# Kernel optimization log

Hardware: AMD Instinct MI355X
Metric: run time of the kernel (lower is better)

The kernel has to match this reference:

```python
import jax, jax.numpy as jnp
import numpy as np

N_DRUG, N_TARGET, N_EDGES, H = 50000, 20000, 500000, 256


def setup_inputs() -> dict:
    key = jax.random.key(0)
    ks = jax.random.split(key, 6)
    s = 1.0 / np.sqrt(2 * H)
    return {
        "z_drug": jax.random.normal(ks[0], (N_DRUG, H), dtype=jnp.float32),
        "z_target": jax.random.normal(ks[1], (N_TARGET, H), dtype=jnp.float32),
        "row": jax.random.randint(ks[2], (N_EDGES,), 0, N_DRUG, dtype=jnp.int64),
        "col": jax.random.randint(ks[3], (N_EDGES,), 0, N_TARGET, dtype=jnp.int64),
        "W1": jax.random.normal(ks[4], (2 * H, H), dtype=jnp.float32) * s,
        "b1": jnp.zeros((H,), dtype=jnp.float32),
        "W2": jax.random.normal(ks[5], (H, 1), dtype=jnp.float32) * (1.0 / np.sqrt(H)),
        "b2": jnp.zeros((1,), dtype=jnp.float32),
    }


def reference(z_drug, z_target, row, col, W1, b1, W2, b2):
    # gather endpoint embeddings by edge index, concat -> [E, 2H]
    zc = jnp.concatenate([z_drug[row], z_target[col]], axis=-1)
    h = jax.nn.relu(zc @ W1 + b1)          # [E, H]
    return h @ W2 + b2                     # [E, 1]
```

## Files before the change

### kernel.cpp

```cpp
#include <hip/hip_runtime.h>
#include <hip/hip_bf16.h>
#include <stdint.h>


typedef unsigned short u16;
typedef __attribute__((ext_vector_type(8))) short short8;
typedef __attribute__((ext_vector_type(4))) float f32x4;

#define HDIM 256
#define KDIM 512
#define BM 128
#define BK 64

__device__ __forceinline__ u16 f2bf(float f) {
  union { float f; uint32_t u; } v; v.f = f;
  uint32_t u = v.u;
  return (u16)((u + 0x7fffu + ((u >> 16) & 1u)) >> 16);
}

__device__ __forceinline__ void gl2lds16(const void* g, void* l) {
  __builtin_amdgcn_global_load_lds(
      (const __attribute__((address_space(1))) unsigned int*)g,
      (__attribute__((address_space(3))) unsigned int*)l,
      16, 0, 0);
}

#define CVT_BLOCKS 4096
__global__ void prep_kernel(const float* __restrict__ zd_f,
                            const float* __restrict__ zt_f,
                            const float* __restrict__ w1,
                            u16* __restrict__ zdb, u16* __restrict__ ztb,
                            u16* __restrict__ w1t, int n4d, int n4t) {
  const int b = blockIdx.x;
  if (b < 32) {
    __shared__ float tile[64][65];
    const int k0 = (b >> 2) * 64, n0 = (b & 3) * 64;
    const int tx = threadIdx.x & 63, ty = threadIdx.x >> 6;
#pragma unroll
    for (int i = ty; i < 64; i += 4)
      tile[i][tx] = w1[(size_t)(k0 + i) * HDIM + n0 + tx];
    __syncthreads();
#pragma unroll
    for (int i = ty; i < 64; i += 4)
      w1t[(size_t)(n0 + i) * KDIM + k0 + tx] = f2bf(tile[tx][i]);
  } else {
    const int idx = (b - 32) * 256 + threadIdx.x;
    const int stride = CVT_BLOCKS * 256;
    for (int i = idx; i < n4d; i += stride) {
      float4 v = ((const float4*)zd_f)[i];
      ushort4 o; o.x = f2bf(v.x); o.y = f2bf(v.y); o.z = f2bf(v.z); o.w = f2bf(v.w);
      ((ushort4*)zdb)[i] = o;
    }
    for (int i = idx; i < n4t; i += stride) {
      float4 v = ((const float4*)zt_f)[i];
      ushort4 o; o.x = f2bf(v.x); o.y = f2bf(v.y); o.z = f2bf(v.z); o.w = f2bf(v.w);
      ((ushort4*)ztb)[i] = o;
    }
  }
}

__global__ __launch_bounds__(256, 2) void edge_mlp_kernel(
    const u16* __restrict__ zd, const u16* __restrict__ zt,
    const int* __restrict__ row, const int* __restrict__ col,
    const u16* __restrict__ w1t, const float* __restrict__ b1,
    const float* __restrict__ w2, const float* __restrict__ b2,
    float* __restrict__ out, int E) {
  __shared__ u16 lB[2][HDIM * BK];

  const int tid   = threadIdx.x;
  const int wid   = tid >> 6;
  const int lane  = tid & 63;
  const int e0    = blockIdx.x * BM;
  const int r8    = lane >> 3;
  const int slog  = ((lane & 7) ^ (r8 & 7)) * 8;
  const int colid = lane & 15;
  const int quad  = lane >> 4;
  const int csw   = colid & 7;

  const u16* pB = w1t + (uint32_t)(wid * 64 + r8) * KDIM + slog;

  uint32_t offD2[2], offT2[2];
#pragma unroll
  for (int rt = 0; rt < 2; ++rt) {
    int ge = min(e0 + wid * 32 + rt * 16 + colid, E - 1);
    offD2[rt] = (uint32_t)row[ge] * HDIM;
    offT2[rt] = (uint32_t)col[ge] * HDIM;
  }

  f32x4 acc[2][16];
#pragma unroll
  for (int i = 0; i < 2; ++i)
#pragma unroll
    for (int j = 0; j < 16; ++j) acc[i][j] = f32x4{0.f, 0.f, 0.f, 0.f};

  short8 aR[2][2][2];

#pragma unroll
  for (int j = 0; j < 8; ++j)
    gl2lds16(pB + (size_t)j * 8 * KDIM, &lB[0][(wid * 64 + j * 8) * BK]);
#pragma unroll
  for (int rt = 0; rt < 2; ++rt)
#pragma unroll
    for (int s = 0; s < 2; ++s)
      aR[0][rt][s] = *(const short8*)(zd + offD2[rt] + s * 32 + quad * 8);
  asm volatile("s_waitcnt vmcnt(0)" ::: "memory");
  __builtin_amdgcn_s_barrier();

#pragma unroll
  for (int kc = 0; kc < 8; ++kc) {
    const int cur = kc & 1, nxt = cur ^ 1;
    if (kc < 7) {
      const int kn = kc + 1;
      const u16* zb = (kn < 4) ? zd : zt;
      const uint32_t* offs = (kn < 4) ? offD2 : offT2;
      const int koffn = (kn & 3) * BK;
#pragma unroll
      for (int j = 0; j < 8; ++j)
        gl2lds16(pB + (size_t)j * 8 * KDIM + kn * BK,
                 &lB[nxt][(wid * 64 + j * 8) * BK]);
#pragma unroll
      for (int rt = 0; rt < 2; ++rt)
#pragma unroll
        for (int s = 0; s < 2; ++s)
          aR[nxt][rt][s] =
              *(const short8*)(zb + offs[rt] + koffn + s * 32 + quad * 8);
    }
#pragma unroll
    for (int s = 0; s < 2; ++s) {
      const int sl = s * 4 + quad;
      __builtin_amdgcn_s_setprio(1);
#pragma unroll
      for (int ct = 0; ct < 16; ++ct) {
        short8 bF = *(const short8*)
            &lB[cur][(ct * 16 + colid) * BK + ((sl ^ csw) * 8)];
        acc[0][ct] = __builtin_amdgcn_mfma_f32_16x16x32_bf16(
            aR[cur][0][s], bF, acc[0][ct], 0, 0, 0);
        acc[1][ct] = __builtin_amdgcn_mfma_f32_16x16x32_bf16(
            aR[cur][1][s], bF, acc[1][ct], 0, 0, 0);
      }
      __builtin_amdgcn_s_setprio(0);
    }
    if (kc < 7) {
      asm volatile("s_waitcnt vmcnt(0)" ::: "memory");
      __builtin_amdgcn_s_barrier();
    }
  }

  float b1v[16], w2v[16];
#pragma unroll
  for (int ct = 0; ct < 16; ++ct) {
    b1v[ct] = b1[ct * 16 + colid];
    w2v[ct] = w2[ct * 16 + colid];
  }
  const float b2v = b2[0];
#pragma unroll
  for (int rt = 0; rt < 2; ++rt)
#pragma unroll
    for (int j = 0; j < 4; ++j) {
      float s = 0.f;
#pragma unroll
      for (int ct = 0; ct < 16; ++ct)
        s += fmaxf(acc[rt][ct][j] + b1v[ct], 0.f) * w2v[ct];
#pragma unroll
      for (int off = 8; off >= 1; off >>= 1)
        s += __shfl_xor(s, off, 16);
      if (colid == 0) {
        int ge = e0 + wid * 32 + rt * 16 + quad * 4 + j;
        if (ge < E) out[ge] = s + b2v;
      }
    }
}

__global__ void fallback_kernel(
    const float* __restrict__ zd, const float* __restrict__ zt,
    const int* __restrict__ row, const int* __restrict__ col,
    const float* __restrict__ W1, const float* __restrict__ b1,
    const float* __restrict__ W2, const float* __restrict__ b2,
    float* __restrict__ out, int E) {
  __shared__ float zc[16][512];
  __shared__ float red[4][16];
  const int e0 = blockIdx.x * 16;
  const int tid = threadIdx.x;
  for (int i = tid; i < 16 * 512; i += 256) {
    int e = i >> 9, k = i & 511;
    int ge = min(e0 + e, E - 1);
    zc[e][k] = (k < HDIM) ? zd[(size_t)row[ge] * HDIM + k]
                          : zt[(size_t)col[ge] * HDIM + (k - HDIM)];
  }
  __syncthreads();
  float acc[16];
#pragma unroll
  for (int e = 0; e < 16; ++e) acc[e] = 0.f;
  for (int k = 0; k < KDIM; ++k) {
    float w = W1[k * HDIM + tid];
#pragma unroll
    for (int e = 0; e < 16; ++e) acc[e] += zc[e][k] * w;
  }
  float wv = W2[tid], bv = b1[tid];
  const int lane = tid & 63, wid = tid >> 6;
#pragma unroll
  for (int e = 0; e < 16; ++e) {
    float pv = fmaxf(acc[e] + bv, 0.f) * wv;
#pragma unroll
    for (int off = 32; off >= 1; off >>= 1) pv += __shfl_down(pv, off, 64);
    if (lane == 0) red[wid][e] = pv;
  }
  __syncthreads();
  if (tid < 16) {
    int ge = e0 + tid;
    if (ge < E)
      out[ge] = red[0][tid] + red[1][tid] + red[2][tid] + red[3][tid] + b2[0];
  }
}

extern "C" void kernel_launch(void* const* d_in, const int* in_sizes, int n_in,
                              void* d_out, int out_size, void* d_ws, size_t ws_size,
                              hipStream_t stream) {
  const float* zd_f = (const float*)d_in[0];
  const float* zt_f = (const float*)d_in[1];
  const int*   row  = (const int*)d_in[2];
  const int*   col  = (const int*)d_in[3];
  const float* W1   = (const float*)d_in[4];
  const float* b1   = (const float*)d_in[5];
  const float* W2   = (const float*)d_in[6];
  const float* b2   = (const float*)d_in[7];
  float* out = (float*)d_out;

  const int E  = in_sizes[2];
  const int ND = in_sizes[0] / HDIM;
  const int NT = in_sizes[1] / HDIM;

  size_t off_w1t = 0;
  size_t off_zd  = (size_t)KDIM * HDIM * sizeof(u16);
  size_t off_zt  = off_zd + (size_t)ND * HDIM * sizeof(u16);
  size_t need    = off_zt + (size_t)NT * HDIM * sizeof(u16);

  if (ws_size >= need) {
    u16* w1t = (u16*)((char*)d_ws + off_w1t);
    u16* zdb = (u16*)((char*)d_ws + off_zd);
    u16* ztb = (u16*)((char*)d_ws + off_zt);
    int n4d = ND * HDIM / 4, n4t = NT * HDIM / 4;
    prep_kernel<<<32 + CVT_BLOCKS, 256, 0, stream>>>(zd_f, zt_f, W1,
                                                     zdb, ztb, w1t, n4d, n4t);
    edge_mlp_kernel<<<(E + BM - 1) / BM, 256, 0, stream>>>(
        zdb, ztb, row, col, w1t, b1, W2, b2, out, E);
  } else {
    fallback_kernel<<<(E + 15) / 16, 256, 0, stream>>>(
        zd_f, zt_f, row, col, W1, b1, W2, b2, out, E);
  }
}
```

Measured before the change: 265.9 us.

## Fuse fp32-to-bf16 embedding conversion into edge MLP gather

Removes the separate pass that converted both embedding tables to bf16 in workspace; the edge kernel now gathers fp32 rows directly and converts to bf16 in registers after the load wait. This eliminates a full read/write sweep of the tables. In exchange, the per-edge gather traffic doubles and more registers are used to hold the fp32 staging values.

```diff
diff --git a/kernel.cpp b/kernel.cpp
--- a/kernel.cpp
+++ b/kernel.cpp
@@ -25,42 +25,23 @@
       16, 0, 0);
 }
 
-#define CVT_BLOCKS 4096
-__global__ void prep_kernel(const float* __restrict__ zd_f,
-                            const float* __restrict__ zt_f,
-                            const float* __restrict__ w1,
-                            u16* __restrict__ zdb, u16* __restrict__ ztb,
-                            u16* __restrict__ w1t, int n4d, int n4t) {
+__global__ void prep_kernel(const float* __restrict__ w1,
+                            u16* __restrict__ w1t) {
   const int b = blockIdx.x;
-  if (b < 32) {
-    __shared__ float tile[64][65];
-    const int k0 = (b >> 2) * 64, n0 = (b & 3) * 64;
-    const int tx = threadIdx.x & 63, ty = threadIdx.x >> 6;
-#pragma unroll
-    for (int i = ty; i < 64; i += 4)
-      tile[i][tx] = w1[(size_t)(k0 + i) * HDIM + n0 + tx];
-    __syncthreads();
-#pragma unroll
-    for (int i = ty; i < 64; i += 4)
-      w1t[(size_t)(n0 + i) * KDIM + k0 + tx] = f2bf(tile[tx][i]);
-  } else {
-    const int idx = (b - 32) * 256 + threadIdx.x;
-    const int stride = CVT_BLOCKS * 256;
-    for (int i = idx; i < n4d; i += stride) {
-      float4 v = ((const float4*)zd_f)[i];
-      ushort4 o; o.x = f2bf(v.x); o.y = f2bf(v.y); o.z = f2bf(v.z); o.w = f2bf(v.w);
-      ((ushort4*)zdb)[i] = o;
-    }
-    for (int i = idx; i < n4t; i += stride) {
-      float4 v = ((const float4*)zt_f)[i];
-      ushort4 o; o.x = f2bf(v.x); o.y = f2bf(v.y); o.z = f2bf(v.z); o.w = f2bf(v.w);
-      ((ushort4*)ztb)[i] = o;
-    }
-  }
+  __shared__ float tile[64][65];
+  const int k0 = (b >> 2) * 64, n0 = (b & 3) * 64;
+  const int tx = threadIdx.x & 63, ty = threadIdx.x >> 6;
+#pragma unroll
+  for (int i = ty; i < 64; i += 4)
+    tile[i][tx] = w1[(size_t)(k0 + i) * HDIM + n0 + tx];
+  __syncthreads();
+#pragma unroll
+  for (int i = ty; i < 64; i += 4)
+    w1t[(size_t)(n0 + i) * KDIM + k0 + tx] = f2bf(tile[tx][i]);
 }
 
 __global__ __launch_bounds__(256, 2) void edge_mlp_kernel(
-    const u16* __restrict__ zd, const u16* __restrict__ zt,
+    const float* __restrict__ zdf, const float* __restrict__ ztf,
     const int* __restrict__ row, const int* __restrict__ col,
     const u16* __restrict__ w1t, const float* __restrict__ b1,
     const float* __restrict__ w2, const float* __restrict__ b2,
@@ -93,17 +74,43 @@
 #pragma unroll
     for (int j = 0; j < 16; ++j) acc[i][j] = f32x4{0.f, 0.f, 0.f, 0.f};
 
-  short8 aR[2][2][2];
+  float4 a32[2][2][2];
+  short8 aB[2][2];
+
+  auto loadA = [&](int kn) {
+    const float* zb = (kn < 4) ? zdf : ztf;
+    const uint32_t* offs = (kn < 4) ? offD2 : offT2;
+    const int koffn = (kn & 3) * BK;
+#pragma unroll
+    for (int rt = 0; rt < 2; ++rt)
+#pragma unroll
+      for (int s = 0; s < 2; ++s) {
+        const float* p = zb + offs[rt] + koffn + s * 32 + quad * 8;
+        a32[rt][s][0] = ((const float4*)p)[0];
+        a32[rt][s][1] = ((const float4*)p)[1];
+      }
+  };
+  auto cvtA = [&]() {
+#pragma unroll
+    for (int rt = 0; rt < 2; ++rt)
+#pragma unroll
+      for (int s = 0; s < 2; ++s) {
+        float4 lo = a32[rt][s][0], hi = a32[rt][s][1];
+        short8 r;
+        r[0] = (short)f2bf(lo.x); r[1] = (short)f2bf(lo.y);
+        r[2] = (short)f2bf(lo.z); r[3] = (short)f2bf(lo.w);
+        r[4] = (short)f2bf(hi.x); r[5] = (short)f2bf(hi.y);
+        r[6] = (short)f2bf(hi.z); r[7] = (short)f2bf(hi.w);
+        aB[rt][s] = r;
+      }
+  };
 
 #pragma unroll
   for (int j = 0; j < 8; ++j)
     gl2lds16(pB + (size_t)j * 8 * KDIM, &lB[0][(wid * 64 + j * 8) * BK]);
-#pragma unroll
-  for (int rt = 0; rt < 2; ++rt)
-#pragma unroll
-    for (int s = 0; s < 2; ++s)
-      aR[0][rt][s] = *(const short8*)(zd + offD2[rt] + s * 32 + quad * 8);
+  loadA(0);
   asm volatile("s_waitcnt vmcnt(0)" ::: "memory");
+  cvtA();
   __builtin_amdgcn_s_barrier();
 
 #pragma unroll
@@ -111,19 +118,11 @@
     const int cur = kc & 1, nxt = cur ^ 1;
     if (kc < 7) {
       const int kn = kc + 1;
-      const u16* zb = (kn < 4) ? zd : zt;
-      const uint32_t* offs = (kn < 4) ? offD2 : offT2;
-      const int koffn = (kn & 3) * BK;
 #pragma unroll
       for (int j = 0; j < 8; ++j)
         gl2lds16(pB + (size_t)j * 8 * KDIM + kn * BK,
                  &lB[nxt][(wid * 64 + j * 8) * BK]);
-#pragma unroll
-      for (int rt = 0; rt < 2; ++rt)
-#pragma unroll
-        for (int s = 0; s < 2; ++s)
-          aR[nxt][rt][s] =
-              *(const short8*)(zb + offs[rt] + koffn + s * 32 + quad * 8);
+      loadA(kn);
     }
 #pragma unroll
     for (int s = 0; s < 2; ++s) {
@@ -134,14 +133,15 @@
         short8 bF = *(const short8*)
             &lB[cur][(ct * 16 + colid) * BK + ((sl ^ csw) * 8)];
         acc[0][ct] = __builtin_amdgcn_mfma_f32_16x16x32_bf16(
-            aR[cur][0][s], bF, acc[0][ct], 0, 0, 0);
+            aB[0][s], bF, acc[0][ct], 0, 0, 0);
         acc[1][ct] = __builtin_amdgcn_mfma_f32_16x16x32_bf16(
-            aR[cur][1][s], bF, acc[1][ct], 0, 0, 0);
+            aB[1][s], bF, acc[1][ct], 0, 0, 0);
       }
       __builtin_amdgcn_s_setprio(0);
     }
     if (kc < 7) {
       asm volatile("s_waitcnt vmcnt(0)" ::: "memory");
+      cvtA();
       __builtin_amdgcn_s_barrier();
     }
   }
@@ -226,24 +226,15 @@
   const float* b2   = (const float*)d_in[7];
   float* out = (float*)d_out;
 
-  const int E  = in_sizes[2];
-  const int ND = in_sizes[0] / HDIM;
-  const int NT = in_sizes[1] / HDIM;
-
-  size_t off_w1t = 0;
-  size_t off_zd  = (size_t)KDIM * HDIM * sizeof(u16);
-  size_t off_zt  = off_zd + (size_t)ND * HDIM * sizeof(u16);
-  size_t need    = off_zt + (size_t)NT * HDIM * sizeof(u16);
+  const int E = in_sizes[2];
+
+  size_t need = (size_t)KDIM * HDIM * sizeof(u16);
 
   if (ws_size >= need) {
-    u16* w1t = (u16*)((char*)d_ws + off_w1t);
-    u16* zdb = (u16*)((char*)d_ws + off_zd);
-    u16* ztb = (u16*)((char*)d_ws + off_zt);
-    int n4d = ND * HDIM / 4, n4t = NT * HDIM / 4;
-    prep_kernel<<<32 + CVT_BLOCKS, 256, 0, stream>>>(zd_f, zt_f, W1,
-                                                     zdb, ztb, w1t, n4d, n4t);
+    u16* w1t = (u16*)d_ws;
+    prep_kernel<<<32, 256, 0, stream>>>(W1, w1t);
     edge_mlp_kernel<<<(E + BM - 1) / BM, 256, 0, stream>>>(
-        zdb, ztb, row, col, w1t, b1, W2, b2, out, E);
+        zd_f, zt_f, row, col, w1t, b1, W2, b2, out, E);
   } else {
     fallback_kernel<<<(E + 15) / 16, 256, 0, stream>>>(
         zd_f, zt_f, row, col, W1, b1, W2, b2, out, E);
```

Result: slower. 313.4 us (+17.9%).

## Split hidden dimension across two blocks per edge group with atomic output reduction

Applied to the files above, without the earlier changes.

Each 128-edge group is now handled by two blocks, each computing half of the 256 hidden units, and the partial dot products with W2 are combined by atomicAdd into an output that is zeroed with a memset first. This halves accumulator registers and LDS per block, raising launch bounds to 3 blocks per SM for more occupancy and more blocks in flight. In exchange, the gathered A rows are loaded twice, and an extra memset plus atomics are added.

```diff
diff --git a/kernel.cpp b/kernel.cpp
--- a/kernel.cpp
+++ b/kernel.cpp
@@ -9,7 +9,7 @@
 
 #define HDIM 256
 #define KDIM 512
-#define BM 128
+#define EG 128
 #define BK 64
 
 __device__ __forceinline__ u16 f2bf(float f) {
@@ -59,25 +59,30 @@
   }
 }
 
-__global__ __launch_bounds__(256, 2) void edge_mlp_kernel(
+__global__ __launch_bounds__(256, 3) void edge_mlp_kernel(
     const u16* __restrict__ zd, const u16* __restrict__ zt,
     const int* __restrict__ row, const int* __restrict__ col,
     const u16* __restrict__ w1t, const float* __restrict__ b1,
     const float* __restrict__ w2, const float* __restrict__ b2,
     float* __restrict__ out, int E) {
-  __shared__ u16 lB[2][HDIM * BK];
+  __shared__ u16 lB[2][128 * BK];
 
   const int tid   = threadIdx.x;
   const int wid   = tid >> 6;
   const int lane  = tid & 63;
-  const int e0    = blockIdx.x * BM;
+  const int g     = blockIdx.x >> 1;
+  const int h     = blockIdx.x & 1;
+  const int e0    = g * EG;
+  const int n0    = h * 128;
   const int r8    = lane >> 3;
   const int slog  = ((lane & 7) ^ (r8 & 7)) * 8;
   const int colid = lane & 15;
   const int quad  = lane >> 4;
   const int csw   = colid & 7;
 
-  const u16* pB = w1t + (uint32_t)(wid * 64 + r8) * KDIM + slog;
+  const u16* pB = w1t + (uint32_t)(n0 + wid * 32 + r8) * KDIM + slog;
+  u16* lBw0 = &lB[0][(wid * 32) * BK];
+  u16* lBw1 = &lB[1][(wid * 32) * BK];
 
   uint32_t offD2[2], offT2[2];
 #pragma unroll
@@ -87,17 +92,17 @@
     offT2[rt] = (uint32_t)col[ge] * HDIM;
   }
 
-  f32x4 acc[2][16];
+  f32x4 acc[2][8];
 #pragma unroll
   for (int i = 0; i < 2; ++i)
 #pragma unroll
-    for (int j = 0; j < 16; ++j) acc[i][j] = f32x4{0.f, 0.f, 0.f, 0.f};
+    for (int j = 0; j < 8; ++j) acc[i][j] = f32x4{0.f, 0.f, 0.f, 0.f};
 
   short8 aR[2][2][2];
 
 #pragma unroll
-  for (int j = 0; j < 8; ++j)
-    gl2lds16(pB + (size_t)j * 8 * KDIM, &lB[0][(wid * 64 + j * 8) * BK]);
+  for (int t = 0; t < 4; ++t)
+    gl2lds16(pB + (size_t)t * 8 * KDIM, lBw0 + t * 8 * BK);
 #pragma unroll
   for (int rt = 0; rt < 2; ++rt)
 #pragma unroll
@@ -111,14 +116,14 @@
     const int cur = kc & 1, nxt = cur ^ 1;
     if (kc < 7) {
       const int kn = kc + 1;
+#pragma unroll
+      for (int t = 0; t < 4; ++t)
+        gl2lds16(pB + (size_t)t * 8 * KDIM + kn * BK,
+                 (nxt ? lBw1 : lBw0) + t * 8 * BK);
       const u16* zb = (kn < 4) ? zd : zt;
       const uint32_t* offs = (kn < 4) ? offD2 : offT2;
       const int koffn = (kn & 3) * BK;
 #pragma unroll
-      for (int j = 0; j < 8; ++j)
-        gl2lds16(pB + (size_t)j * 8 * KDIM + kn * BK,
-                 &lB[nxt][(wid * 64 + j * 8) * BK]);
-#pragma unroll
       for (int rt = 0; rt < 2; ++rt)
 #pragma unroll
         for (int s = 0; s < 2; ++s)
@@ -130,7 +135,7 @@
       const int sl = s * 4 + quad;
       __builtin_amdgcn_s_setprio(1);
 #pragma unroll
-      for (int ct = 0; ct < 16; ++ct) {
+      for (int ct = 0; ct < 8; ++ct) {
         short8 bF = *(const short8*)
             &lB[cur][(ct * 16 + colid) * BK + ((sl ^ csw) * 8)];
         acc[0][ct] = __builtin_amdgcn_mfma_f32_16x16x32_bf16(
@@ -146,27 +151,28 @@
     }
   }
 
-  float b1v[16], w2v[16];
-#pragma unroll
-  for (int ct = 0; ct < 16; ++ct) {
-    b1v[ct] = b1[ct * 16 + colid];
-    w2v[ct] = w2[ct * 16 + colid];
-  }
-  const float b2v = b2[0];
+  float b1v[8], w2v[8];
+#pragma unroll
+  for (int ct = 0; ct < 8; ++ct) {
+    int n = n0 + ct * 16 + colid;
+    b1v[ct] = b1[n];
+    w2v[ct] = w2[n];
+  }
+  const float badd = (h == 0) ? b2[0] : 0.f;
 #pragma unroll
   for (int rt = 0; rt < 2; ++rt)
 #pragma unroll
     for (int j = 0; j < 4; ++j) {
       float s = 0.f;
 #pragma unroll
-      for (int ct = 0; ct < 16; ++ct)
+      for (int ct = 0; ct < 8; ++ct)
         s += fmaxf(acc[rt][ct][j] + b1v[ct], 0.f) * w2v[ct];
 #pragma unroll
       for (int off = 8; off >= 1; off >>= 1)
         s += __shfl_xor(s, off, 16);
       if (colid == 0) {
         int ge = e0 + wid * 32 + rt * 16 + quad * 4 + j;
-        if (ge < E) out[ge] = s + b2v;
+        if (ge < E) atomicAdd(&out[ge], s + badd);
       }
     }
 }
@@ -242,7 +248,9 @@
     int n4d = ND * HDIM / 4, n4t = NT * HDIM / 4;
     prep_kernel<<<32 + CVT_BLOCKS, 256, 0, stream>>>(zd_f, zt_f, W1,
                                                      zdb, ztb, w1t, n4d, n4t);
-    edge_mlp_kernel<<<(E + BM - 1) / BM, 256, 0, stream>>>(
+    hipMemsetAsync(out, 0, (size_t)E * sizeof(float), stream);
+    const int nG = (E + EG - 1) / EG;
+    edge_mlp_kernel<<<nG * 2, 256, 0, stream>>>(
         zdb, ztb, row, col, w1t, b1, W2, b2, out, E);
   } else {
     fallback_kernel<<<(E + 15) / 16, 256, 0, stream>>>(
```

Result: slower. 275.1 us (+3.5%).
